# Kernel optimization log

Measured on AMD Instinct MI355X. Metric: run time of the kernel, lower is better.

The kernel has to match this reference:

```python
import jax, jax.numpy as jnp
import numpy as np

N_NODES = 50000
DIM_IN = 256
DIM_OUT = 256
N_EDGES = 1600000


def setup_inputs() -> dict:
    key = jax.random.key(0)
    k1, k2, k3, k4, k5 = jax.random.split(key, 5)
    feature = jax.random.normal(k1, (N_NODES, DIM_IN), dtype=jnp.float32)
    src = jax.random.randint(k2, (N_EDGES,), 0, N_NODES, dtype=jnp.int32)
    dst = jax.random.randint(k3, (N_EDGES,), 0, N_NODES, dtype=jnp.int32)
    # Linear(dim_in, dim_out) params
    bound = 1.0 / np.sqrt(DIM_IN)
    W = jax.random.uniform(k4, (DIM_OUT, DIM_IN), dtype=jnp.float32, minval=-bound, maxval=bound)
    b = jax.random.uniform(k5, (DIM_OUT,), dtype=jnp.float32, minval=-bound, maxval=bound)
    return {"feature": feature, "src": src, "dst": dst, "W": W, "b": b}


def reference(feature, src, dst, W, b):
    # copy_u: gather source features per edge; mean-reduce per destination node.
    msg_sum = jax.ops.segment_sum(feature[src], dst, num_segments=N_NODES)  # [N, Din]
    deg = jax.ops.segment_sum(jnp.ones((src.shape[0],), feature.dtype), dst,
                              num_segments=N_NODES)  # [N]
    mean = msg_sum / jnp.maximum(deg, 1.0)[:, None]
    # DGL update_all only overwrites 'h' for nodes that received messages;
    # isolated (in-degree 0) nodes keep their original feature.
    h = jnp.where((deg > 0)[:, None], mean, feature)
    # apply_nodes: Linear on all nodes
    return h @ W.T + b
```

## Files before the change

### kernel.cpp

```cpp
#include <hip/hip_runtime.h>
#include <hip/hip_bf16.h>

#define N_NODES 50000
#define NPAD 50016
#define DUMMY 50000
#define DIM 256
#define N_EDGES 1600000
#define NBUK 196
#define CAP 10240
#define CHUNK_E 4096
#define NBLK ((N_EDGES + CHUNK_E - 1) / CHUNK_E)
#define GEMM_BLKS ((N_NODES + 63) / 64)
#define NCHUNK 8
#define AGG_BPC 782
#define NGROUP (N_NODES / 16)
#define LROW 72

typedef float f32x4 __attribute__((ext_vector_type(4)));
typedef __bf16 bf16x8 __attribute__((ext_vector_type(8)));
typedef __bf16 bf16x4 __attribute__((ext_vector_type(4)));
typedef unsigned long long u64;
typedef unsigned int u32;
typedef unsigned short u16;

__global__ __launch_bounds__(256) void prep_k(const float* __restrict__ W,
                                              __bf16* __restrict__ Wbf,
                                              __bf16* __restrict__ Yc,
                                              const int* __restrict__ src,
                                              const int* __restrict__ dst,
                                              int* __restrict__ bcur,
                                              unsigned int* __restrict__ staged) {
    __shared__ int lh[NBUK];
    __shared__ int lbase[NBUK];

    if (blockIdx.x < NBLK) {
        int pb = blockIdx.x;
        for (int i = threadIdx.x; i < NBUK; i += 256) lh[i] = 0;
        __syncthreads();
        int base = pb * CHUNK_E;
        int end = base + CHUNK_E; if (end > N_EDGES) end = N_EDGES;
        for (int e = base + threadIdx.x; e < end; e += 256)
            atomicAdd(&lh[dst[e] >> 8], 1);
        __syncthreads();
        for (int i = threadIdx.x; i < NBUK; i += 256) {
            int c = lh[i];
            lbase[i] = c ? (atomicAdd(&bcur[i], c) + i * CAP) : 0;
            lh[i] = 0;
        }
        __syncthreads();
        for (int e = base + threadIdx.x; e < end; e += 256) {
            int d = dst[e];
            int s = src[e];
            int b = d >> 8;
            int p = atomicAdd(&lh[b], 1);
            staged[lbase[b] + p] = (unsigned int)s | ((unsigned int)(d & 255) << 16);
        }
    } else {
        int p = blockIdx.x - NBLK;
        if (p < 256) {
            int i = p * 256 + threadIdx.x;
            Wbf[i] = (__bf16)W[i];
        } else {
            for (int i = threadIdx.x; i < NCHUNK * 16 * 32; i += 256) {
                int c = i >> 9;
                int rem = i & 511;
                Yc[(size_t)c * NPAD * 32 + (size_t)(N_NODES + (rem >> 5)) * 32 + (rem & 31)]
                    = (__bf16)0.0f;
            }
        }
    }
}

__global__ __launch_bounds__(256) void gemmfin_k(const float* __restrict__ feat,
                                                 const __bf16* __restrict__ Wbf,
                                                 __bf16* __restrict__ Yc,
                                                 const unsigned int* __restrict__ staged,
                                                 const int* __restrict__ bcur,
                                                 int* __restrict__ offs,
                                                 u16* __restrict__ deg16,
                                                 u16* __restrict__ edge16) {
    __shared__ __bf16 lw[256 * LROW];
    __shared__ int nh[256];
    __shared__ int nbase[256];
    __shared__ int sm[256];

    if (blockIdx.x < GEMM_BLKS) {
        const int wid  = threadIdx.x >> 6;
        const int lane = threadIdx.x & 63;
        const int row0 = blockIdx.x * 64 + wid * 16;
        const int mrow = lane & 15;
        const int kgrp = lane >> 4;

        int arow = row0 + mrow;
        int arow_c = arow < N_NODES ? arow : (N_NODES - 1);
        const float* aptr = feat + (size_t)arow_c * DIM + kgrp * 8;

        const int t = threadIdx.x;
        const int srow = t >> 3;
        const int scb  = (t & 7) * 8;

        f32x4 acc[16];
#pragma unroll
        for (int i = 0; i < 16; ++i) acc[i] = (f32x4)0.0f;

        for (int p = 0; p < 4; ++p) {
            f32x4 ar0 = *(const f32x4*)(aptr + (p * 2) * 32);
            f32x4 ar1 = *(const f32x4*)(aptr + (p * 2) * 32 + 4);
            f32x4 ar2 = *(const f32x4*)(aptr + (p * 2 + 1) * 32);
            f32x4 ar3 = *(const f32x4*)(aptr + (p * 2 + 1) * 32 + 4);

            if (p) __syncthreads();
#pragma unroll
            for (int i = 0; i < 8; ++i) {
                int row = srow + i * 32;
                uint4 v = *(const uint4*)(Wbf + (size_t)row * DIM + p * 64 + scb);
                *(uint4*)(lw + row * LROW + scb) = v;
            }
            __syncthreads();

            bf16x8 af0, af1;
            af0[0] = (__bf16)ar0[0]; af0[1] = (__bf16)ar0[1];
            af0[2] = (__bf16)ar0[2]; af0[3] = (__bf16)ar0[3];
            af0[4] = (__bf16)ar1[0]; af0[5] = (__bf16)ar1[1];
            af0[6] = (__bf16)ar1[2]; af0[7] = (__bf16)ar1[3];
            af1[0] = (__bf16)ar2[0]; af1[1] = (__bf16)ar2[1];
            af1[2] = (__bf16)ar2[2]; af1[3] = (__bf16)ar2[3];
            af1[4] = (__bf16)ar3[0]; af1[5] = (__bf16)ar3[1];
            af1[6] = (__bf16)ar3[2]; af1[7] = (__bf16)ar3[3];

#pragma unroll
            for (int nt = 0; nt < 16; ++nt) {
                const __bf16* lp = lw + (nt * 16 + mrow) * LROW + kgrp * 8;
                bf16x8 wf0 = *(const bf16x8*)(lp);
                bf16x8 wf1 = *(const bf16x8*)(lp + 32);
                acc[nt] = __builtin_amdgcn_mfma_f32_16x16x32_bf16(wf0, af0, acc[nt], 0, 0, 0);
                acc[nt] = __builtin_amdgcn_mfma_f32_16x16x32_bf16(wf1, af1, acc[nt], 0, 0, 0);
            }
        }

        const int node = row0 + mrow;
        if (node < N_NODES) {
#pragma unroll
            for (int nt = 0; nt < 16; ++nt) {
                int oc0 = nt * 16 + kgrp * 4;
                bf16x4 pv;
                pv[0] = (__bf16)acc[nt][0];
                pv[1] = (__bf16)acc[nt][1];
                pv[2] = (__bf16)acc[nt][2];
                pv[3] = (__bf16)acc[nt][3];
                __bf16* yp = Yc + (size_t)(oc0 >> 5) * NPAD * 32
                                + (size_t)node * 32 + (oc0 & 31);
                *(bf16x4*)yp = pv;
            }
        }
    } else {
        int t = threadIdx.x, b = blockIdx.x - GEMM_BLKS;
        int beg = b * CAP;
        int cnt = bcur[b];
        nh[t] = 0;
        __syncthreads();
        for (int i = t; i < cnt; i += 256)
            atomicAdd(&nh[staged[beg + i] >> 16], 1);
        __syncthreads();
        int v = nh[t];
        int v8 = (v + 7) & ~7;
        sm[t] = v8;
        __syncthreads();
        for (int off = 1; off < 256; off <<= 1) {
            int x = (t >= off) ? sm[t - off] : 0;
            __syncthreads();
            sm[t] += x;
            __syncthreads();
        }
        nbase[t] = sm[t] - v8;
        int node = (b << 8) + t;
        if (node < N_NODES) {
            offs[node]  = beg + nbase[t];
            deg16[node] = (u16)v;
        }
        for (int i = v; i < v8; ++i)
            edge16[beg + nbase[t] + i] = (u16)DUMMY;
        nh[t] = 0;
        __syncthreads();
        for (int i = t; i < cnt; i += 256) {
            unsigned int u = staged[beg + i];
            int dl = (int)(u >> 16);
            int p = atomicAdd(&nh[dl], 1);
            edge16[beg + nbase[dl] + p] = (u16)(u & 0xFFFFu);
        }
    }
}

#define GQ(ev) (*(const uint4*)(Ybase + (size_t)((u32)(ev) & 0xffffu) * 32 + cl))
#define ACCQ(q) do { \
    a0 += __uint_as_float((q).x << 16); a1 += __uint_as_float((q).x); \
    a2 += __uint_as_float((q).y << 16); a3 += __uint_as_float((q).y); \
    a4 += __uint_as_float((q).z << 16); a5 += __uint_as_float((q).z); \
    a6 += __uint_as_float((q).w << 16); a7 += __uint_as_float((q).w); \
} while (0)

__global__ __launch_bounds__(256) void aggregate_k(const __bf16* __restrict__ Yc,
                                                   const int* __restrict__ offs,
                                                   const u16* __restrict__ deg16,
                                                   const u16* __restrict__ edge16,
                                                   const float* __restrict__ bias,
                                                   float* __restrict__ out) {
    const int chunk = blockIdx.x & 7;
    const int bic   = blockIdx.x >> 3;
    const int wid   = threadIdx.x >> 6;
    const int lane  = threadIdx.x & 63;
    const int seg   = lane >> 2;
    const int cl    = (lane & 3) * 8;

    const int g = bic * 4 + wid;
    if (g >= NGROUP) return;
    const int node = g * 16 + seg;

    const __bf16* Ybase = Yc + (size_t)chunk * NPAD * 32;
    const float* bp = bias + chunk * 32 + cl;
    const f32x4 bv0 = *(const f32x4*)bp;
    const f32x4 bv1 = *(const f32x4*)(bp + 4);

    const int beg = offs[node];
    const int dg  = (int)deg16[node];

    float a0 = 0.f, a1 = 0.f, a2 = 0.f, a3 = 0.f;
    float a4 = 0.f, a5 = 0.f, a6 = 0.f, a7 = 0.f;

    f32x4 r0, r1;
    if (dg > 0) {
        const int nb8 = (dg + 7) >> 3;
        const int npair = nb8 >> 1;
        const int odd = nb8 & 1;
        int j = beg;
        u64 eA = *(const u64*)(edge16 + j);
        u64 eB = *(const u64*)(edge16 + j + 4);
        u64 eC = *(const u64*)(edge16 + j + 8);
        u64 eD = *(const u64*)(edge16 + j + 12);
        for (int p = 0; p < npair; ++p) {
            u64 nA = *(const u64*)(edge16 + j + 16);
            u64 nB = *(const u64*)(edge16 + j + 20);
            u64 nC = *(const u64*)(edge16 + j + 24);
            u64 nD = *(const u64*)(edge16 + j + 28);
            uint4 q0 = GQ(eA);       uint4 q1 = GQ(eA >> 16);
            uint4 q2 = GQ(eA >> 32); uint4 q3 = GQ(eA >> 48);
            uint4 q4 = GQ(eB);       uint4 q5 = GQ(eB >> 16);
            uint4 q6 = GQ(eB >> 32); uint4 q7 = GQ(eB >> 48);
            uint4 q8 = GQ(eC);       uint4 q9 = GQ(eC >> 16);
            uint4 qa = GQ(eC >> 32); uint4 qb = GQ(eC >> 48);
            uint4 qc = GQ(eD);       uint4 qd = GQ(eD >> 16);
            uint4 qe = GQ(eD >> 32); uint4 qf = GQ(eD >> 48);
            __builtin_amdgcn_sched_barrier(0);
            ACCQ(q0); ACCQ(q1); ACCQ(q2); ACCQ(q3);
            ACCQ(q4); ACCQ(q5); ACCQ(q6); ACCQ(q7);
            ACCQ(q8); ACCQ(q9); ACCQ(qa); ACCQ(qb);
            ACCQ(qc); ACCQ(qd); ACCQ(qe); ACCQ(qf);
            j += 16;
            eA = nA; eB = nB; eC = nC; eD = nD;
        }
        if (odd) {
            uint4 q0 = GQ(eA);       uint4 q1 = GQ(eA >> 16);
            uint4 q2 = GQ(eA >> 32); uint4 q3 = GQ(eA >> 48);
            uint4 q4 = GQ(eB);       uint4 q5 = GQ(eB >> 16);
            uint4 q6 = GQ(eB >> 32); uint4 q7 = GQ(eB >> 48);
            ACCQ(q0); ACCQ(q1); ACCQ(q2); ACCQ(q3);
            ACCQ(q4); ACCQ(q5); ACCQ(q6); ACCQ(q7);
        }
        float inv = 1.0f / (float)dg;
        r0[0] = a0 * inv + bv0[0];
        r0[1] = a1 * inv + bv0[1];
        r0[2] = a2 * inv + bv0[2];
        r0[3] = a3 * inv + bv0[3];
        r1[0] = a4 * inv + bv1[0];
        r1[1] = a5 * inv + bv1[1];
        r1[2] = a6 * inv + bv1[2];
        r1[3] = a7 * inv + bv1[3];
    } else {
        uint4 q = *(const uint4*)(Ybase + (size_t)node * 32 + cl);
        r0[0] = __uint_as_float(q.x << 16) + bv0[0];
        r0[1] = __uint_as_float(q.x & 0xffff0000u) + bv0[1];
        r0[2] = __uint_as_float(q.y << 16) + bv0[2];
        r0[3] = __uint_as_float(q.y & 0xffff0000u) + bv0[3];
        r1[0] = __uint_as_float(q.z << 16) + bv1[0];
        r1[1] = __uint_as_float(q.z & 0xffff0000u) + bv1[1];
        r1[2] = __uint_as_float(q.w << 16) + bv1[2];
        r1[3] = __uint_as_float(q.w & 0xffff0000u) + bv1[3];
    }
    float* op = out + (size_t)node * DIM + chunk * 32 + cl;
    *(f32x4*)op = r0;
    *(f32x4*)(op + 4) = r1;
}

static inline size_t align64(size_t x) { return (x + 63) & ~(size_t)63; }

extern "C" void kernel_launch(void* const* d_in, const int* in_sizes, int n_in,
                              void* d_out, int out_size, void* d_ws, size_t ws_size,
                              hipStream_t stream) {
    const float* feature = (const float*)d_in[0];
    const int*   src     = (const int*)d_in[1];
    const int*   dst     = (const int*)d_in[2];
    const float* W       = (const float*)d_in[3];
    const float* b       = (const float*)d_in[4];
    float* out = (float*)d_out;

    char* ws = (char*)d_ws;
    __bf16* Yc  = (__bf16*)ws;               ws += align64((size_t)NCHUNK * NPAD * 32 * 2);
    __bf16* Wbf = (__bf16*)ws;               ws += align64((size_t)DIM * DIM * 2);
    int* offs     = (int*)ws;                ws += align64((size_t)N_NODES * 4);
    u16* deg16    = (u16*)ws;                ws += align64((size_t)N_NODES * 2);
    int* bcur     = (int*)ws;                ws += align64((size_t)NBUK * 4);
    unsigned int* staged = (unsigned int*)ws; ws += align64((size_t)NBUK * CAP * 4);
    u16* edge16   = (u16*)ws;                ws += align64((size_t)NBUK * CAP * 2 + 128);

    hipMemsetAsync(bcur, 0, (size_t)NBUK * 4, stream);
    prep_k<<<NBLK + 257, 256, 0, stream>>>(W, Wbf, Yc, src, dst, bcur, staged);
    gemmfin_k<<<GEMM_BLKS + NBUK, 256, 0, stream>>>(feature, Wbf, Yc, staged, bcur,
                                                    offs, deg16, edge16);
    aggregate_k<<<NCHUNK * AGG_BPC, 256, 0, stream>>>(Yc, offs, deg16, edge16, b, out);
}
```

Before: 144.7 us.

## Sort nodes by in-degree for balanced aggregation and fuse GEMM into bucketing kernel

Moves the bf16 GEMM into the first kernel next to edge bucketing, converting W from fp32 on the fly, and drops the separate Wbf conversion pass. Finalization becomes its own kernel that also builds a degree histogram. A scan and scatter then produce a permutation of nodes sorted by degree, and aggregation processes nodes through that permutation so each 16-node group has similar degree and less divergence. This adds two small launches and an indirect load per node, and removes a sched_barrier from the gather loop.

```diff
diff --git a/kernel.cpp b/kernel.cpp
--- a/kernel.cpp
+++ b/kernel.cpp
@@ -15,6 +15,7 @@
 #define AGG_BPC 782
 #define NGROUP (N_NODES / 16)
 #define LROW 72
+#define NBIN 256
 
 typedef float f32x4 __attribute__((ext_vector_type(4)));
 typedef __bf16 bf16x8 __attribute__((ext_vector_type(8)));
@@ -23,15 +24,16 @@
 typedef unsigned int u32;
 typedef unsigned short u16;
 
-__global__ __launch_bounds__(256) void prep_k(const float* __restrict__ W,
-                                              __bf16* __restrict__ Wbf,
-                                              __bf16* __restrict__ Yc,
-                                              const int* __restrict__ src,
-                                              const int* __restrict__ dst,
-                                              int* __restrict__ bcur,
-                                              unsigned int* __restrict__ staged) {
-    __shared__ int lh[NBUK];
-    __shared__ int lbase[NBUK];
+__global__ __launch_bounds__(256) void k1_k(const float* __restrict__ feat,
+                                            const float* __restrict__ W,
+                                            __bf16* __restrict__ Yc,
+                                            const int* __restrict__ src,
+                                            const int* __restrict__ dst,
+                                            int* __restrict__ bcur,
+                                            unsigned int* __restrict__ staged) {
+    __shared__ __bf16 lw[256 * LROW];
+    int* lh    = (int*)lw;
+    int* lbase = lh + NBUK;
 
     if (blockIdx.x < NBLK) {
         int pb = blockIdx.x;
@@ -56,11 +58,22 @@
             staged[lbase[b] + p] = (unsigned int)s | ((unsigned int)(d & 255) << 16);
         }
     } else {
-        int p = blockIdx.x - NBLK;
-        if (p < 256) {
-            int i = p * 256 + threadIdx.x;
-            Wbf[i] = (__bf16)W[i];
-        } else {
+        const int gb   = blockIdx.x - NBLK;
+        const int wid  = threadIdx.x >> 6;
+        const int lane = threadIdx.x & 63;
+        const int row0 = gb * 64 + wid * 16;
+        const int mrow = lane & 15;
+        const int kgrp = lane >> 4;
+
+        int arow = row0 + mrow;
+        int arow_c = arow < N_NODES ? arow : (N_NODES - 1);
+        const float* aptr = feat + (size_t)arow_c * DIM + kgrp * 8;
+
+        const int t = threadIdx.x;
+        const int srow = t >> 3;
+        const int scb  = (t & 7) * 8;
+
+        if (gb == 0) {
             for (int i = threadIdx.x; i < NCHUNK * 16 * 32; i += 256) {
                 int c = i >> 9;
                 int rem = i & 511;
@@ -68,36 +81,6 @@
                     = (__bf16)0.0f;
             }
         }
-    }
-}
-
-__global__ __launch_bounds__(256) void gemmfin_k(const float* __restrict__ feat,
-                                                 const __bf16* __restrict__ Wbf,
-                                                 __bf16* __restrict__ Yc,
-                                                 const unsigned int* __restrict__ staged,
-                                                 const int* __restrict__ bcur,
-                                                 int* __restrict__ offs,
-                                                 u16* __restrict__ deg16,
-                                                 u16* __restrict__ edge16) {
-    __shared__ __bf16 lw[256 * LROW];
-    __shared__ int nh[256];
-    __shared__ int nbase[256];
-    __shared__ int sm[256];
-
-    if (blockIdx.x < GEMM_BLKS) {
-        const int wid  = threadIdx.x >> 6;
-        const int lane = threadIdx.x & 63;
-        const int row0 = blockIdx.x * 64 + wid * 16;
-        const int mrow = lane & 15;
-        const int kgrp = lane >> 4;
-
-        int arow = row0 + mrow;
-        int arow_c = arow < N_NODES ? arow : (N_NODES - 1);
-        const float* aptr = feat + (size_t)arow_c * DIM + kgrp * 8;
-
-        const int t = threadIdx.x;
-        const int srow = t >> 3;
-        const int scb  = (t & 7) * 8;
 
         f32x4 acc[16];
 #pragma unroll
@@ -113,8 +96,15 @@
 #pragma unroll
             for (int i = 0; i < 8; ++i) {
                 int row = srow + i * 32;
-                uint4 v = *(const uint4*)(Wbf + (size_t)row * DIM + p * 64 + scb);
-                *(uint4*)(lw + row * LROW + scb) = v;
+                const float* wp = W + (size_t)row * DIM + p * 64 + scb;
+                f32x4 w0 = *(const f32x4*)(wp);
+                f32x4 w1 = *(const f32x4*)(wp + 4);
+                bf16x8 wv;
+                wv[0] = (__bf16)w0[0]; wv[1] = (__bf16)w0[1];
+                wv[2] = (__bf16)w0[2]; wv[3] = (__bf16)w0[3];
+                wv[4] = (__bf16)w1[0]; wv[5] = (__bf16)w1[1];
+                wv[6] = (__bf16)w1[2]; wv[7] = (__bf16)w1[3];
+                *(bf16x8*)(lw + row * LROW + scb) = wv;
             }
             __syncthreads();
 
@@ -153,41 +143,99 @@
                 *(bf16x4*)yp = pv;
             }
         }
-    } else {
-        int t = threadIdx.x, b = blockIdx.x - GEMM_BLKS;
-        int beg = b * CAP;
-        int cnt = bcur[b];
-        nh[t] = 0;
-        __syncthreads();
-        for (int i = t; i < cnt; i += 256)
-            atomicAdd(&nh[staged[beg + i] >> 16], 1);
-        __syncthreads();
-        int v = nh[t];
-        int v8 = (v + 7) & ~7;
-        sm[t] = v8;
-        __syncthreads();
-        for (int off = 1; off < 256; off <<= 1) {
-            int x = (t >= off) ? sm[t - off] : 0;
-            __syncthreads();
-            sm[t] += x;
-            __syncthreads();
-        }
-        nbase[t] = sm[t] - v8;
-        int node = (b << 8) + t;
-        if (node < N_NODES) {
-            offs[node]  = beg + nbase[t];
-            deg16[node] = (u16)v;
-        }
-        for (int i = v; i < v8; ++i)
-            edge16[beg + nbase[t] + i] = (u16)DUMMY;
-        nh[t] = 0;
-        __syncthreads();
-        for (int i = t; i < cnt; i += 256) {
-            unsigned int u = staged[beg + i];
-            int dl = (int)(u >> 16);
-            int p = atomicAdd(&nh[dl], 1);
-            edge16[beg + nbase[dl] + p] = (u16)(u & 0xFFFFu);
-        }
+    }
+}
+
+__global__ __launch_bounds__(256) void finalize_k(const unsigned int* __restrict__ staged,
+                                                  const int* __restrict__ bcur,
+                                                  int* __restrict__ offs,
+                                                  u16* __restrict__ deg16,
+                                                  u16* __restrict__ edge16,
+                                                  int* __restrict__ degbin) {
+    __shared__ int nh[256];
+    __shared__ int nbase[256];
+    __shared__ int sm[256];
+    __shared__ int dh[NBIN];
+    int t = threadIdx.x, b = blockIdx.x;
+    int beg = b * CAP;
+    int cnt = bcur[b];
+    nh[t] = 0;
+    dh[t] = 0;
+    __syncthreads();
+    for (int i = t; i < cnt; i += 256)
+        atomicAdd(&nh[staged[beg + i] >> 16], 1);
+    __syncthreads();
+    int v = nh[t];
+    int v8 = (v + 7) & ~7;
+    sm[t] = v8;
+    __syncthreads();
+    for (int off = 1; off < 256; off <<= 1) {
+        int x = (t >= off) ? sm[t - off] : 0;
+        __syncthreads();
+        sm[t] += x;
+        __syncthreads();
+    }
+    nbase[t] = sm[t] - v8;
+    int node = (b << 8) + t;
+    if (node < N_NODES) {
+        offs[node]  = beg + nbase[t];
+        deg16[node] = (u16)v;
+        int bin = v < NBIN ? v : NBIN - 1;
+        atomicAdd(&dh[bin], 1);
+    }
+    for (int i = v; i < v8; ++i)
+        edge16[beg + nbase[t] + i] = (u16)DUMMY;
+    nh[t] = 0;
+    __syncthreads();
+    if (dh[t]) atomicAdd(&degbin[t], dh[t]);
+    for (int i = t; i < cnt; i += 256) {
+        unsigned int u = staged[beg + i];
+        int dl = (int)(u >> 16);
+        int p = atomicAdd(&nh[dl], 1);
+        edge16[beg + nbase[dl] + p] = (u16)(u & 0xFFFFu);
+    }
+}
+
+__global__ __launch_bounds__(NBIN) void scan_k(const int* __restrict__ degbin,
+                                               int* __restrict__ bincur) {
+    __shared__ int sm[NBIN];
+    int t = threadIdx.x;
+    int v = degbin[t];
+    sm[t] = v;
+    __syncthreads();
+    for (int off = 1; off < NBIN; off <<= 1) {
+        int x = (t >= off) ? sm[t - off] : 0;
+        __syncthreads();
+        sm[t] += x;
+        __syncthreads();
+    }
+    bincur[t] = sm[t] - v;
+}
+
+__global__ __launch_bounds__(256) void scatter_k(const u16* __restrict__ deg16,
+                                                 int* __restrict__ bincur,
+                                                 u16* __restrict__ perm) {
+    __shared__ int dh[NBIN];
+    __shared__ int dbase[NBIN];
+    int t = threadIdx.x;
+    int node = blockIdx.x * 256 + t;
+    int valid = node < N_NODES;
+    dh[t] = 0;
+    __syncthreads();
+    int bin = 0;
+    if (valid) {
+        int v = (int)deg16[node];
+        bin = v < NBIN ? v : NBIN - 1;
+        atomicAdd(&dh[bin], 1);
+    }
+    __syncthreads();
+    int c = dh[t];
+    dbase[t] = c ? atomicAdd(&bincur[t], c) : 0;
+    dh[t] = 0;
+    __syncthreads();
+    if (valid) {
+        int p = atomicAdd(&dh[bin], 1);
+        perm[dbase[bin] + p] = (u16)node;
     }
 }
 
@@ -203,6 +251,7 @@
                                                    const int* __restrict__ offs,
                                                    const u16* __restrict__ deg16,
                                                    const u16* __restrict__ edge16,
+                                                   const u16* __restrict__ perm,
                                                    const float* __restrict__ bias,
                                                    float* __restrict__ out) {
     const int chunk = blockIdx.x & 7;
@@ -214,7 +263,7 @@
 
     const int g = bic * 4 + wid;
     if (g >= NGROUP) return;
-    const int node = g * 16 + seg;
+    const int node = (int)perm[g * 16 + seg];
 
     const __bf16* Ybase = Yc + (size_t)chunk * NPAD * 32;
     const float* bp = bias + chunk * 32 + cl;
@@ -250,7 +299,6 @@
             uint4 qa = GQ(eC >> 32); uint4 qb = GQ(eC >> 48);
             uint4 qc = GQ(eD);       uint4 qd = GQ(eD >> 16);
             uint4 qe = GQ(eD >> 32); uint4 qf = GQ(eD >> 48);
-            __builtin_amdgcn_sched_barrier(0);
             ACCQ(q0); ACCQ(q1); ACCQ(q2); ACCQ(q3);
             ACCQ(q4); ACCQ(q5); ACCQ(q6); ACCQ(q7);
             ACCQ(q8); ACCQ(q9); ACCQ(qa); ACCQ(qb);
@@ -305,16 +353,19 @@
 
     char* ws = (char*)d_ws;
     __bf16* Yc  = (__bf16*)ws;               ws += align64((size_t)NCHUNK * NPAD * 32 * 2);
-    __bf16* Wbf = (__bf16*)ws;               ws += align64((size_t)DIM * DIM * 2);
     int* offs     = (int*)ws;                ws += align64((size_t)N_NODES * 4);
     u16* deg16    = (u16*)ws;                ws += align64((size_t)N_NODES * 2);
-    int* bcur     = (int*)ws;                ws += align64((size_t)NBUK * 4);
+    u16* perm     = (u16*)ws;                ws += align64((size_t)N_NODES * 2);
+    int* bcur     = (int*)ws;
+    int* degbin   = bcur + NBUK;             ws += align64((size_t)(NBUK + NBIN) * 4);
+    int* bincur   = (int*)ws;                ws += align64((size_t)NBIN * 4);
     unsigned int* staged = (unsigned int*)ws; ws += align64((size_t)NBUK * CAP * 4);
     u16* edge16   = (u16*)ws;                ws += align64((size_t)NBUK * CAP * 2 + 128);
 
-    hipMemsetAsync(bcur, 0, (size_t)NBUK * 4, stream);
-    prep_k<<<NBLK + 257, 256, 0, stream>>>(W, Wbf, Yc, src, dst, bcur, staged);
-    gemmfin_k<<<GEMM_BLKS + NBUK, 256, 0, stream>>>(feature, Wbf, Yc, staged, bcur,
-                                                    offs, deg16, edge16);
-    aggregate_k<<<NCHUNK * AGG_BPC, 256, 0, stream>>>(Yc, offs, deg16, edge16, b, out);
-}
+    hipMemsetAsync(bcur, 0, (size_t)(NBUK + NBIN) * 4, stream);
+    k1_k<<<NBLK + GEMM_BLKS, 256, 0, stream>>>(feature, W, Yc, src, dst, bcur, staged);
+    finalize_k<<<NBUK, 256, 0, stream>>>(staged, bcur, offs, deg16, edge16, degbin);
+    scan_k<<<1, NBIN, 0, stream>>>(degbin, bincur);
+    scatter_k<<<NBUK, 256, 0, stream>>>(deg16, bincur, perm);
+    aggregate_k<<<NCHUNK * AGG_BPC, 256, 0, stream>>>(Yc, offs, deg16, edge16, perm, b, out);
+}
```

New measurement: 159.8 us. 10.4% more time.

## Fuse GEMM into bucketing kernel and convert W to bf16 on the fly

Applied to the files above, without the earlier changes.

The dense GEMM moves into the first kernel alongside the edge bucketing blocks, so the two run concurrently. Each GEMM block now converts its W tiles from fp32 to bf16 while loading them, which removes the separate Wbf conversion pass and its buffer. The finalize (CSR build) step becomes its own small kernel, and the sched_barrier in the aggregate loop is removed. The cost is that every GEMM block reads fp32 W, twice the bytes, and the small finalize kernel now runs alone on the critical path.

```diff
diff --git a/kernel.cpp b/kernel.cpp
--- a/kernel.cpp
+++ b/kernel.cpp
@@ -23,15 +23,16 @@
 typedef unsigned int u32;
 typedef unsigned short u16;
 
-__global__ __launch_bounds__(256) void prep_k(const float* __restrict__ W,
-                                              __bf16* __restrict__ Wbf,
-                                              __bf16* __restrict__ Yc,
-                                              const int* __restrict__ src,
-                                              const int* __restrict__ dst,
-                                              int* __restrict__ bcur,
-                                              unsigned int* __restrict__ staged) {
-    __shared__ int lh[NBUK];
-    __shared__ int lbase[NBUK];
+__global__ __launch_bounds__(256) void k1_k(const float* __restrict__ feat,
+                                            const float* __restrict__ W,
+                                            __bf16* __restrict__ Yc,
+                                            const int* __restrict__ src,
+                                            const int* __restrict__ dst,
+                                            int* __restrict__ bcur,
+                                            unsigned int* __restrict__ staged) {
+    __shared__ __bf16 lw[256 * LROW];
+    int* lh    = (int*)lw;
+    int* lbase = lh + NBUK;
 
     if (blockIdx.x < NBLK) {
         int pb = blockIdx.x;
@@ -56,11 +57,22 @@
             staged[lbase[b] + p] = (unsigned int)s | ((unsigned int)(d & 255) << 16);
         }
     } else {
-        int p = blockIdx.x - NBLK;
-        if (p < 256) {
-            int i = p * 256 + threadIdx.x;
-            Wbf[i] = (__bf16)W[i];
-        } else {
+        const int gb   = blockIdx.x - NBLK;
+        const int wid  = threadIdx.x >> 6;
+        const int lane = threadIdx.x & 63;
+        const int row0 = gb * 64 + wid * 16;
+        const int mrow = lane & 15;
+        const int kgrp = lane >> 4;
+
+        int arow = row0 + mrow;
+        int arow_c = arow < N_NODES ? arow : (N_NODES - 1);
+        const float* aptr = feat + (size_t)arow_c * DIM + kgrp * 8;
+
+        const int t = threadIdx.x;
+        const int srow = t >> 3;
+        const int scb  = (t & 7) * 8;
+
+        if (gb == 0) {
             for (int i = threadIdx.x; i < NCHUNK * 16 * 32; i += 256) {
                 int c = i >> 9;
                 int rem = i & 511;
@@ -68,36 +80,6 @@
                     = (__bf16)0.0f;
             }
         }
-    }
-}
-
-__global__ __launch_bounds__(256) void gemmfin_k(const float* __restrict__ feat,
-                                                 const __bf16* __restrict__ Wbf,
-                                                 __bf16* __restrict__ Yc,
-                                                 const unsigned int* __restrict__ staged,
-                                                 const int* __restrict__ bcur,
-                                                 int* __restrict__ offs,
-                                                 u16* __restrict__ deg16,
-                                                 u16* __restrict__ edge16) {
-    __shared__ __bf16 lw[256 * LROW];
-    __shared__ int nh[256];
-    __shared__ int nbase[256];
-    __shared__ int sm[256];
-
-    if (blockIdx.x < GEMM_BLKS) {
-        const int wid  = threadIdx.x >> 6;
-        const int lane = threadIdx.x & 63;
-        const int row0 = blockIdx.x * 64 + wid * 16;
-        const int mrow = lane & 15;
-        const int kgrp = lane >> 4;
-
-        int arow = row0 + mrow;
-        int arow_c = arow < N_NODES ? arow : (N_NODES - 1);
-        const float* aptr = feat + (size_t)arow_c * DIM + kgrp * 8;
-
-        const int t = threadIdx.x;
-        const int srow = t >> 3;
-        const int scb  = (t & 7) * 8;
 
         f32x4 acc[16];
 #pragma unroll
@@ -113,8 +95,15 @@
 #pragma unroll
             for (int i = 0; i < 8; ++i) {
                 int row = srow + i * 32;
-                uint4 v = *(const uint4*)(Wbf + (size_t)row * DIM + p * 64 + scb);
-                *(uint4*)(lw + row * LROW + scb) = v;
+                const float* wp = W + (size_t)row * DIM + p * 64 + scb;
+                f32x4 w0 = *(const f32x4*)(wp);
+                f32x4 w1 = *(const f32x4*)(wp + 4);
+                bf16x8 wv;
+                wv[0] = (__bf16)w0[0]; wv[1] = (__bf16)w0[1];
+                wv[2] = (__bf16)w0[2]; wv[3] = (__bf16)w0[3];
+                wv[4] = (__bf16)w1[0]; wv[5] = (__bf16)w1[1];
+                wv[6] = (__bf16)w1[2]; wv[7] = (__bf16)w1[3];
+                *(bf16x8*)(lw + row * LROW + scb) = wv;
             }
             __syncthreads();
 
@@ -153,41 +142,50 @@
                 *(bf16x4*)yp = pv;
             }
         }
-    } else {
-        int t = threadIdx.x, b = blockIdx.x - GEMM_BLKS;
-        int beg = b * CAP;
-        int cnt = bcur[b];
-        nh[t] = 0;
-        __syncthreads();
-        for (int i = t; i < cnt; i += 256)
-            atomicAdd(&nh[staged[beg + i] >> 16], 1);
-        __syncthreads();
-        int v = nh[t];
-        int v8 = (v + 7) & ~7;
-        sm[t] = v8;
-        __syncthreads();
-        for (int off = 1; off < 256; off <<= 1) {
-            int x = (t >= off) ? sm[t - off] : 0;
-            __syncthreads();
-            sm[t] += x;
-            __syncthreads();
-        }
-        nbase[t] = sm[t] - v8;
-        int node = (b << 8) + t;
-        if (node < N_NODES) {
-            offs[node]  = beg + nbase[t];
-            deg16[node] = (u16)v;
-        }
-        for (int i = v; i < v8; ++i)
-            edge16[beg + nbase[t] + i] = (u16)DUMMY;
-        nh[t] = 0;
-        __syncthreads();
-        for (int i = t; i < cnt; i += 256) {
-            unsigned int u = staged[beg + i];
-            int dl = (int)(u >> 16);
-            int p = atomicAdd(&nh[dl], 1);
-            edge16[beg + nbase[dl] + p] = (u16)(u & 0xFFFFu);
-        }
+    }
+}
+
+__global__ __launch_bounds__(256) void finalize_k(const unsigned int* __restrict__ staged,
+                                                  const int* __restrict__ bcur,
+                                                  int* __restrict__ offs,
+                                                  u16* __restrict__ deg16,
+                                                  u16* __restrict__ edge16) {
+    __shared__ int nh[256];
+    __shared__ int nbase[256];
+    __shared__ int sm[256];
+    int t = threadIdx.x, b = blockIdx.x;
+    int beg = b * CAP;
+    int cnt = bcur[b];
+    nh[t] = 0;
+    __syncthreads();
+    for (int i = t; i < cnt; i += 256)
+        atomicAdd(&nh[staged[beg + i] >> 16], 1);
+    __syncthreads();
+    int v = nh[t];
+    int v8 = (v + 7) & ~7;
+    sm[t] = v8;
+    __syncthreads();
+    for (int off = 1; off < 256; off <<= 1) {
+        int x = (t >= off) ? sm[t - off] : 0;
+        __syncthreads();
+        sm[t] += x;
+        __syncthreads();
+    }
+    nbase[t] = sm[t] - v8;
+    int node = (b << 8) + t;
+    if (node < N_NODES) {
+        offs[node]  = beg + nbase[t];
+        deg16[node] = (u16)v;
+    }
+    for (int i = v; i < v8; ++i)
+        edge16[beg + nbase[t] + i] = (u16)DUMMY;
+    nh[t] = 0;
+    __syncthreads();
+    for (int i = t; i < cnt; i += 256) {
+        unsigned int u = staged[beg + i];
+        int dl = (int)(u >> 16);
+        int p = atomicAdd(&nh[dl], 1);
+        edge16[beg + nbase[dl] + p] = (u16)(u & 0xFFFFu);
     }
 }
 
@@ -250,7 +248,6 @@
             uint4 qa = GQ(eC >> 32); uint4 qb = GQ(eC >> 48);
             uint4 qc = GQ(eD);       uint4 qd = GQ(eD >> 16);
             uint4 qe = GQ(eD >> 32); uint4 qf = GQ(eD >> 48);
-            __builtin_amdgcn_sched_barrier(0);
             ACCQ(q0); ACCQ(q1); ACCQ(q2); ACCQ(q3);
             ACCQ(q4); ACCQ(q5); ACCQ(q6); ACCQ(q7);
             ACCQ(q8); ACCQ(q9); ACCQ(qa); ACCQ(qb);
@@ -305,7 +302,6 @@
 
     char* ws = (char*)d_ws;
     __bf16* Yc  = (__bf16*)ws;               ws += align64((size_t)NCHUNK * NPAD * 32 * 2);
-    __bf16* Wbf = (__bf16*)ws;               ws += align64((size_t)DIM * DIM * 2);
     int* offs     = (int*)ws;                ws += align64((size_t)N_NODES * 4);
     u16* deg16    = (u16*)ws;                ws += align64((size_t)N_NODES * 2);
     int* bcur     = (int*)ws;                ws += align64((size_t)NBUK * 4);
@@ -313,8 +309,7 @@
     u16* edge16   = (u16*)ws;                ws += align64((size_t)NBUK * CAP * 2 + 128);
 
     hipMemsetAsync(bcur, 0, (size_t)NBUK * 4, stream);
-    prep_k<<<NBLK + 257, 256, 0, stream>>>(W, Wbf, Yc, src, dst, bcur, staged);
-    gemmfin_k<<<GEMM_BLKS + NBUK, 256, 0, stream>>>(feature, Wbf, Yc, staged, bcur,
-                                                    offs, deg16, edge16);
+    k1_k<<<NBLK + GEMM_BLKS, 256, 0, stream>>>(feature, W, Yc, src, dst, bcur, staged);
+    finalize_k<<<NBUK, 256, 0, stream>>>(staged, bcur, offs, deg16, edge16);
     aggregate_k<<<NCHUNK * AGG_BPC, 256, 0, stream>>>(Yc, offs, deg16, edge16, b, out);
 }
```

Measured after the change: 140.9 us. 2.6% less time.
